# Optimization experiments

Hardware: AMD Instinct MI355X
Metric: run time of the kernel (lower is better)

## Reference

```python
import jax, jax.numpy as jnp
import numpy as np

SHIFT = 7  # shift_size; pad = 3


def _gn(x, w, b, eps=1e-5):
    # GroupNorm(1, C): normalize over (C,H,W) per sample, affine per channel
    m = jnp.mean(x, axis=(1, 2, 3), keepdims=True)
    v = jnp.var(x, axis=(1, 2, 3), keepdims=True)
    return (x - m) * jax.lax.rsqrt(v + eps) * w[None, :, None, None] + b[None, :, None, None]


def _conv1x1(x, w, b):
    return jnp.einsum('bchw,oc->bohw', x, w) + b[None, :, None, None]


def _gelu(x):
    return jax.nn.gelu(x, approximate=False)


def _shift_h(x, size):
    # CUDA kernel semantics: g = c // ceil(C/size); s = -(g - size//2);
    # out[n,c,h,w] = x[n,c,h+s,w] if in-bounds else 0  (dim=2)
    B, C, H, W = x.shape
    pad = size // 2
    group = -(-C // size)  # ceil
    s = pad - (jnp.arange(C) // group)              # [C], values in [-pad, pad]
    xp = jnp.pad(x, ((0, 0), (0, 0), (pad, pad), (0, 0)))
    idx = jnp.arange(H)[None, :] + s[:, None] + pad  # [C,H], in [0, H+2p-1]
    c = jnp.arange(C)[:, None]
    return xp[:, c, idx, :]


def _shift_w(x, size):
    return _shift_h(x.swapaxes(2, 3), size).swapaxes(2, 3)


def _axial_shift(x, c1w, c1b, n1w, n1b, c21w, c21b, c22w, c22b, n2w, n2b, c3w, c3b):
    x = _gelu(_gn(_conv1x1(x, c1w, c1b), n1w, n1b))
    x_lr = _shift_w(x, SHIFT)
    x_td = _shift_h(x, SHIFT)
    x_lr = _gelu(_conv1x1(x_lr, c21w, c21b))
    x_td = _gelu(_conv1x1(x_td, c22w, c22b))
    x = _gn(x_lr + x_td, n2w, n2b)
    return _conv1x1(x, c3w, c3b)


def setup_inputs() -> dict:
    B, C, H, W = 16, 256, 56, 56
    HID = 4 * C
    key = jax.random.key(0)
    ks = jax.random.split(key, 8)
    wscale = 0.05
    inp = {
        'x': jax.random.normal(ks[0], (B, C, H, W), jnp.float32),
        'n1_w': jnp.ones((C,), jnp.float32), 'n1_b': jnp.zeros((C,), jnp.float32),
        'as_c1_w': jax.random.normal(ks[1], (C, C), jnp.float32) * wscale,
        'as_c1_b': jnp.zeros((C,), jnp.float32),
        'as_n1_w': jnp.ones((C,), jnp.float32), 'as_n1_b': jnp.zeros((C,), jnp.float32),
        'as_c21_w': jax.random.normal(ks[2], (C, C), jnp.float32) * wscale,
        'as_c21_b': jnp.zeros((C,), jnp.float32),
        'as_c22_w': jax.random.normal(ks[3], (C, C), jnp.float32) * wscale,
        'as_c22_b': jnp.zeros((C,), jnp.float32),
        'as_n2_w': jnp.ones((C,), jnp.float32), 'as_n2_b': jnp.zeros((C,), jnp.float32),
        'as_c3_w': jax.random.normal(ks[4], (C, C), jnp.float32) * wscale,
        'as_c3_b': jnp.zeros((C,), jnp.float32),
        'n2_w': jnp.ones((C,), jnp.float32), 'n2_b': jnp.zeros((C,), jnp.float32),
        'fc1_w': jax.random.normal(ks[5], (HID, C), jnp.float32) * wscale,
        'fc1_b': jnp.zeros((HID,), jnp.float32),
        'fc2_w': jax.random.normal(ks[6], (C, HID), jnp.float32) * wscale,
        'fc2_b': jnp.zeros((C,), jnp.float32),
    }
    return inp


def reference(x, n1_w, n1_b, as_c1_w, as_c1_b, as_n1_w, as_n1_b,
              as_c21_w, as_c21_b, as_c22_w, as_c22_b, as_n2_w, as_n2_b,
              as_c3_w, as_c3_b, n2_w, n2_b, fc1_w, fc1_b, fc2_w, fc2_b):
    # AxialShiftedBlock: x = x + AxialShift(norm1(x)); x = x + Mlp(norm2(x))
    h = _gn(x, n1_w, n1_b)
    h = _axial_shift(h, as_c1_w, as_c1_b, as_n1_w, as_n1_b,
                     as_c21_w, as_c21_b, as_c22_w, as_c22_b,
                     as_n2_w, as_n2_b, as_c3_w, as_c3_b)
    x = x + h
    h = _gn(x, n2_w, n2_b)
    h = _gelu(_conv1x1(h, fc1_w, fc1_b))
    h = _conv1x1(h, fc2_w, fc2_b)
    return x + h
```

## Files before the change

### kernel.cpp

```cpp
#include <hip/hip_runtime.h>

typedef __attribute__((ext_vector_type(4))) float f32x4;
typedef __attribute__((ext_vector_type(8))) short bf16x8;
typedef __attribute__((ext_vector_type(4))) unsigned short u16x4;
typedef unsigned short u16;

#define HW 3136
#define NSEG 49
#define NELF 802816.0f
#define EPS 1e-5f

__device__ __forceinline__ short f2bf(float f) {
  union { float f; unsigned u; } v; v.f = f;
  unsigned r = (v.u + 0x7FFFu + ((v.u >> 16) & 1u)) >> 16;
  return (short)r;
}
__device__ __forceinline__ float b2f(u16 u) {
  union { unsigned u; float f; } v; v.u = ((unsigned)u) << 16;
  return v.f;
}
__device__ __forceinline__ float fgelu(float x) {
  float x2 = x * x;
  float u = x * (0.7978845608f + 0.0356774081f * x2);
  float e = __expf(-2.0f * u);
  return x * __builtin_amdgcn_rcpf(1.0f + e);
}
__device__ __forceinline__ void gload16(const void* g, void* l) {
  __builtin_amdgcn_global_load_lds(
      (const __attribute__((address_space(1))) void*)(uintptr_t)g,
      (__attribute__((address_space(3))) void*)(unsigned)(uintptr_t)l,
      16, 0, 0);
}

__global__ void wfold_kernel(const float* __restrict__ c1, const float* __restrict__ c21,
                             const float* __restrict__ c22, const float* __restrict__ c3,
                             const float* __restrict__ fc1, const float* __restrict__ fc2,
                             const float* __restrict__ n1w, const float* __restrict__ an2w,
                             const float* __restrict__ n2w, u16* __restrict__ out) {
  int i = (blockIdx.x * 256 + threadIdx.x) * 4;
  const float* src; int off; const float* scale = nullptr;
  if (i < 65536)       { src = c1;  off = 0;       scale = n1w; }
  else if (i < 131072) { src = c21; off = 65536; }
  else if (i < 196608) { src = c22; off = 131072; }
  else if (i < 262144) { src = c3;  off = 196608;  scale = an2w; }
  else if (i < 524288) { src = fc1; off = 262144;  scale = n2w; }
  else                 { src = fc2; off = 524288; }
  int li = i - off;
  float4 v = *(const float4*)(src + li);
  if (scale) {
    float4 g = *(const float4*)(scale + (li & 255));
    v.x *= g.x; v.y *= g.y; v.z *= g.z; v.w *= g.w;
  }
  u16x4 o4; o4[0] = (u16)f2bf(v.x); o4[1] = (u16)f2bf(v.y); o4[2] = (u16)f2bf(v.z); o4[3] = (u16)f2bf(v.w);
  *(u16x4*)(out + i) = o4;
}

__global__ void rowsum_kernel(const float* __restrict__ c1w, const float* __restrict__ c1b,
                              const float* __restrict__ n1w, const float* __restrict__ n1b,
                              const float* __restrict__ c3w, const float* __restrict__ c3b,
                              const float* __restrict__ an2w, const float* __restrict__ an2b,
                              const float* __restrict__ fc1w, const float* __restrict__ fc1b,
                              const float* __restrict__ n2w, const float* __restrict__ n2b,
                              float* __restrict__ sums) {
  int o = blockIdx.x * 256 + threadIdx.x;
  const float *W, *gw, *gb, *cb; float *Sg, *Sb; int row;
  if (o < 256)      { W = c1w;  gw = n1w;  gb = n1b;  cb = c1b;  Sg = sums;        Sb = sums + 256;  row = o; }
  else if (o < 512) { W = c3w;  gw = an2w; gb = an2b; cb = c3b;  Sg = sums + 512;  Sb = sums + 768;  row = o - 256; }
  else              { W = fc1w; gw = n2w;  gb = n2b;  cb = fc1b; Sg = sums + 1024; Sb = sums + 2048; row = o - 512; }
  float sg = 0.f, sb = 0.f;
  for (int c = 0; c < 256; c += 4) {
    float4 w = *(const float4*)(W + (size_t)row * 256 + c);
    float4 g = *(const float4*)(gw + c);
    float4 b = *(const float4*)(gb + c);
    sg += w.x * g.x + w.y * g.y + w.z * g.z + w.w * g.w;
    sb += w.x * b.x + w.y * b.y + w.z * b.z + w.w * b.w;
  }
  Sg[row] = sg; Sb[row] = sb + cb[row];
}

__global__ __launch_bounds__(256) void t0_kernel(const float* __restrict__ x,
                                                 u16* __restrict__ xT, float* __restrict__ st) {
  __shared__ __align__(16) u16 tile[64 * 256];
  const int t = threadIdx.x;
  const int n = blockIdx.x / NSEG;
  const int hw0 = (blockIdx.x % NSEG) * 64;
  const int pix = t & 63;
  float s = 0.f, q = 0.f;
#pragma unroll
  for (int r = 0; r < 16; ++r) {
    int cq = (t >> 6) + (r << 2);
    int c = cq * 4;
    u16x4 o4;
#pragma unroll
    for (int i = 0; i < 4; ++i) {
      float v = x[((size_t)n * 256 + c + i) * HW + hw0 + pix];
      s += v; q += v * v;
      o4[i] = (u16)f2bf(v);
    }
    int u = cq ^ ((pix & 15) << 2);
    *(u16x4*)((char*)tile + pix * 512 + u * 8) = o4;
  }
  __syncthreads();
  {
    const int p2 = t >> 2;
#pragma unroll
    for (int r = 0; r < 8; ++r) {
      int oct = (t & 3) + (r << 2);
      int up = (2 * oct) ^ ((p2 & 15) << 2);
      bf16x8 v = *(const bf16x8*)((char*)tile + p2 * 512 + up * 8);
      *(bf16x8*)&xT[((size_t)n * HW + hw0 + p2) * 256 + oct * 8] = v;
    }
  }
  __syncthreads();
  float* red = (float*)tile;
  red[t] = s; red[256 + t] = q;
  __syncthreads();
  for (int off = 128; off > 0; off >>= 1) {
    if (t < off) { red[t] += red[t + off]; red[256 + t] += red[256 + t + off]; }
    __syncthreads();
  }
  if (t == 0) { atomicAdd(&st[n * 2], red[0]); atomicAdd(&st[n * 2 + 1], red[256]); }
}

__global__ void e2_kernel(const u16* __restrict__ y, u16* __restrict__ tb,
                          const float* __restrict__ gw, const float* __restrict__ gb,
                          const float* __restrict__ stats) {
  const size_t NG = (size_t)16 * HW * 32;
  for (size_t g = (size_t)blockIdx.x * blockDim.x + threadIdx.x; g < NG;
       g += (size_t)gridDim.x * blockDim.x) {
    size_t base = g * 8;
    int n = (int)(base / 802816);
    int c0 = (int)(base & 255);
    float sm = stats[n * 2], sq = stats[n * 2 + 1];
    float mn = sm * (1.0f / NELF);
    float rstd = rsqrtf(sq * (1.0f / NELF) - mn * mn + EPS);
    bf16x8 v = *(const bf16x8*)(y + base);
    bf16x8 o;
#pragma unroll
    for (int j = 0; j < 8; ++j) {
      float sc = rstd * gw[c0 + j];
      float sh = gb[c0 + j] - mn * sc;
      o[j] = f2bf(fgelu(b2f((u16)v[j]) * sc + sh));
    }
    *(bf16x8*)(tb + base) = o;
  }
}

template<int EPI>
__global__ __launch_bounds__(512, 2) void gemmW2(
    const u16* __restrict__ actT, const u16* __restrict__ wt,
    const float* __restrict__ Sg, const float* __restrict__ Sb,
    const float* __restrict__ stats_in, float* __restrict__ stats_out,
    const u16* __restrict__ residCL, u16* __restrict__ outT)
{
  __shared__ __align__(16) u16 lds[79872];
  const int t = threadIdx.x;
  const int lane = t & 63, wave = t >> 6;
  const int fr = lane & 15, fq = lane >> 4;
  const int wo = wave >> 1, wp = wave & 1;
  const int n = blockIdx.x / 14;
  const int hw0 = (blockIdx.x % 14) * 224;
  const size_t nHW = (size_t)n * HW;

  {
    int u0 = t, u1 = t + 512;
    int r0 = u0 >> 2, sg0 = ((u0 & 3) - (r0 >> 1)) & 3;
    int r1 = u1 >> 2, sg1 = ((u1 & 3) - (r1 >> 1)) & 3;
    const u16* w0 = wt + (size_t)r0 * 256 + sg0 * 8;
    const u16* w1 = wt + (size_t)r1 * 256 + sg1 * 8;
#pragma unroll
    for (int k = 0; k < 8; ++k) {
      gload16(w0 + k * 32, &lds[k * 8192 + wave * 512]);
      gload16(w1 + k * 32, &lds[k * 8192 + 4096 + wave * 512]);
    }
  }

  int aU[4], bO[7];
#pragma unroll
  for (int os = 0; os < 4; ++os) { int row = wo * 64 + os * 16 + fr; aU[os] = (4 * row + ((fq + (row >> 1)) & 3)) * 8; }
#pragma unroll
  for (int ps = 0; ps < 7; ++ps) bO[ps] = (fq * 224 + wp * 112 + ps * 16 + fr) * 8;

  auto stageB = [&](int par, int ks) {
    if (wave < 7) {
#pragma unroll
      for (int i = 0; i < 2; ++i) {
        int ub = wave * 128 + i * 64;
        int u = ub + lane;
        int j = u / 224, p = u - j * 224;
        gload16(actT + (nHW + hw0 + p) * 256 + ks * 32 + j * 8,
                &lds[65536 + par * 7168 + ub * 8]);
      }
    }
  };

  f32x4 acc[4][7];
#pragma unroll
  for (int a = 0; a < 4; ++a)
#pragma unroll
    for (int b = 0; b < 7; ++b) acc[a][b] = (f32x4){0.f, 0.f, 0.f, 0.f};

  stageB(0, 0);
  __syncthreads();

#pragma unroll
  for (int k = 0; k < 8; ++k) {
    if (k < 7) stageB((k + 1) & 1, k + 1);
    bf16x8 afr[4], bfr[7];
#pragma unroll
    for (int os = 0; os < 4; ++os) afr[os] = *(const bf16x8*)&lds[k * 8192 + aU[os]];
#pragma unroll
    for (int ps = 0; ps < 7; ++ps) bfr[ps] = *(const bf16x8*)&lds[65536 + (k & 1) * 7168 + bO[ps]];
#pragma unroll
    for (int os = 0; os < 4; ++os)
#pragma unroll
      for (int ps = 0; ps < 7; ++ps)
        acc[os][ps] = __builtin_amdgcn_mfma_f32_16x16x32_bf16(afr[os], bfr[ps], acc[os][ps], 0, 0, 0);
    __syncthreads();
  }

  char* tl = (char*)lds;
  float sm = stats_in[n * 2], sq = stats_in[n * 2 + 1];
  float mn = sm * (1.0f / NELF);
  float rstd = rsqrtf(sq * (1.0f / NELF) - mn * mn + EPS);
  float mr = mn * rstd;
  float lsum = 0.f, lsq = 0.f;
#pragma unroll
  for (int os = 0; os < 4; ++os) {
    const int ob = wo * 64 + os * 16 + fq * 4;
    float4 g4 = *(const float4*)&Sg[ob];
    float4 s4 = *(const float4*)&Sb[ob];
    float be[4] = {s4.x - mr * g4.x, s4.y - mr * g4.y, s4.z - mr * g4.z, s4.w - mr * g4.w};
#pragma unroll
    for (int ps = 0; ps < 7; ++ps) {
      const int pix = wp * 112 + ps * 16 + fr;
      u16x4 rv = {0, 0, 0, 0};
      if (EPI == 1) rv = *(const u16x4*)&residCL[(nHW + hw0 + pix) * 256 + ob];
      u16x4 pk;
#pragma unroll
      for (int j = 0; j < 4; ++j) {
        float v = fmaf(acc[os][ps][j], rstd, be[j]);
        if (EPI == 1) v += b2f(rv[j]);
        lsum += v; lsq += v * v;
        pk[j] = (u16)f2bf(v);
      }
      const int qd = wo * 16 + os * 4 + fq;
      const int uq = qd ^ ((pix & 15) << 2);
      *(u16x4*)(tl + pix * 512 + uq * 8) = pk;
    }
  }
  __syncthreads();
#pragma unroll
  for (int r = 0; r < 14; ++r) {
    int idx = t + r * 512;
    int pix = idx >> 5, oct = idx & 31;
    int up = (2 * oct) ^ ((pix & 15) << 2);
    bf16x8 v = *(const bf16x8*)(tl + pix * 512 + up * 8);
    *(bf16x8*)&outT[(nHW + hw0 + pix) * 256 + oct * 8] = v;
  }
  __syncthreads();
  float* red = (float*)lds;
  red[t] = lsum; red[512 + t] = lsq;
  __syncthreads();
  for (int off = 256; off > 0; off >>= 1) {
    if (t < off) { red[t] += red[t + off]; red[512 + t] += red[512 + t + off]; }
    __syncthreads();
  }
  if (t == 0) { atomicAdd(&stats_out[n * 2], red[0]); atomicAdd(&stats_out[n * 2 + 1], red[512]); }
}

__global__ __launch_bounds__(512, 2) void gemm_dual4(
    const u16* __restrict__ tT, const u16* __restrict__ w21, const u16* __restrict__ w22,
    const float* __restrict__ b21, const float* __restrict__ b22,
    float* __restrict__ stats_out, u16* __restrict__ zT)
{
  __shared__ __align__(16) u16 lds[47616];
  const int t = threadIdx.x;
  const int lane = t & 63, wave = t >> 6;
  const int fr = lane & 15, fq = lane >> 4;
  const int n = blockIdx.x / 28;
  const int hw0 = (blockIdx.x % 28) * 112;
  const size_t nHW = (size_t)n * HW;

  const int u = (t < 448) ? t : 447;
  const int jl = u / 112, p = u - jl * 112;
  const int pix = hw0 + p;
  const int wc = pix % 56, hc = pix / 56;

  bf16x8 gA0, gA1, gB0, gB1;
  auto gatherIssue = [&](int ks) {
    int c0 = ks * 32 + jl * 8;
    int g0 = c0 / 37;
    int s0 = 3 - g0;
    int pa0 = pix + s0;           pa0 = pa0 < 0 ? 0 : (pa0 > HW - 1 ? HW - 1 : pa0);
    int pa1 = pix + s0 - 1;       pa1 = pa1 < 0 ? 0 : (pa1 > HW - 1 ? HW - 1 : pa1);
    int pb0 = pix + 56 * s0;      pb0 = pb0 < 0 ? 0 : (pb0 > HW - 1 ? HW - 1 : pb0);
    int pb1 = pix + 56 * (s0 - 1); pb1 = pb1 < 0 ? 0 : (pb1 > HW - 1 ? HW - 1 : pb1);
    gA0 = *(const bf16x8*)(tT + (nHW + pa0) * 256 + c0);
    gA1 = *(const bf16x8*)(tT + (nHW + pa1) * 256 + c0);
    gB0 = *(const bf16x8*)(tT + (nHW + pb0) * 256 + c0);
    gB1 = *(const bf16x8*)(tT + (nHW + pb1) * 256 + c0);
  };
  auto gatherWrite = [&](int par, int ks) {
    int c0 = ks * 32 + jl * 8;
    int g0 = c0 / 37;
    int s0 = 3 - g0;
    int js = (g0 + 1) * 37 - c0; if (js > 8) js = 8;
    bool a0 = (unsigned)(wc + s0) < 56u, a1 = (unsigned)(wc + s0 - 1) < 56u;
    bool b0 = (unsigned)(hc + s0) < 56u, b1 = (unsigned)(hc + s0 - 1) < 56u;
    bf16x8 va, vb;
#pragma unroll
    for (int j = 0; j < 8; ++j) {
      bool lo = j < js;
      va[j] = lo ? (a0 ? gA0[j] : (short)0) : (a1 ? gA1[j] : (short)0);
      vb[j] = lo ? (b0 ? gB0[j] : (short)0) : (b1 ? gB1[j] : (short)0);
    }
    if (t < 448) {
      *(bf16x8*)&lds[32768 + par * 3712 + (jl * 116 + p) * 8] = va;
      *(bf16x8*)&lds[40192 + par * 3712 + (jl * 116 + p) * 8] = vb;
    }
  };
  auto stageW = [&](int par, int ks) {
    int u0 = t; int r0 = u0 >> 2, sg0 = ((u0 & 3) - (r0 >> 1)) & 3;
    int u1 = t + 512; int r1 = u1 >> 2, sg1 = ((u1 & 3) - (r1 >> 1)) & 3;
    gload16(w21 + (size_t)r0 * 256 + ks * 32 + sg0 * 8, &lds[par * 8192 + wave * 512]);
    gload16(w21 + (size_t)r1 * 256 + ks * 32 + sg1 * 8, &lds[par * 8192 + 4096 + wave * 512]);
    gload16(w22 + (size_t)r0 * 256 + ks * 32 + sg0 * 8, &lds[16384 + par * 8192 + wave * 512]);
    gload16(w22 + (size_t)r1 * 256 + ks * 32 + sg1 * 8, &lds[16384 + par * 8192 + 4096 + wave * 512]);
  };

  int aU[2], bP[7];
#pragma unroll
  for (int os = 0; os < 2; ++os) { int row = wave * 32 + os * 16 + fr; aU[os] = (4 * row + ((fq + (row >> 1)) & 3)) * 8; }
#pragma unroll
  for (int ps = 0; ps < 7; ++ps) bP[ps] = (fq * 116 + ps * 16 + fr) * 8;

  f32x4 accA[2][7], accB[2][7];
#pragma unroll
  for (int a = 0; a < 2; ++a)
#pragma unroll
    for (int b = 0; b < 7; ++b) { accA[a][b] = (f32x4){0, 0, 0, 0}; accB[a][b] = (f32x4){0, 0, 0, 0}; }

  gatherIssue(0);
  stageW(0, 0);
  gatherWrite(0, 0);
  gatherIssue(1);
  __syncthreads();

#pragma unroll
  for (int k = 0; k < 8; ++k) {
    if (k < 7) stageW((k + 1) & 1, k + 1);
    bf16x8 afA[2], afB[2], bfA[7], bfB[7];
#pragma unroll
    for (int os = 0; os < 2; ++os) {
      afA[os] = *(const bf16x8*)&lds[(k & 1) * 8192 + aU[os]];
      afB[os] = *(const bf16x8*)&lds[16384 + (k & 1) * 8192 + aU[os]];
    }
#pragma unroll
    for (int ps = 0; ps < 7; ++ps) {
      bfA[ps] = *(const bf16x8*)&lds[32768 + (k & 1) * 3712 + bP[ps]];
      bfB[ps] = *(const bf16x8*)&lds[40192 + (k & 1) * 3712 + bP[ps]];
    }
#pragma unroll
    for (int os = 0; os < 2; ++os)
#pragma unroll
      for (int ps = 0; ps < 7; ++ps) {
        accA[os][ps] = __builtin_amdgcn_mfma_f32_16x16x32_bf16(afA[os], bfA[ps], accA[os][ps], 0, 0, 0);
        accB[os][ps] = __builtin_amdgcn_mfma_f32_16x16x32_bf16(afB[os], bfB[ps], accB[os][ps], 0, 0, 0);
      }
    if (k < 7) {
      gatherWrite((k + 1) & 1, k + 1);
      if (k < 6) gatherIssue(k + 2);
    }
    __syncthreads();
  }

  char* tl = (char*)lds;
  float lsum = 0.f, lsq = 0.f;
#pragma unroll
  for (int os = 0; os < 2; ++os) {
    const int ob = wave * 32 + os * 16 + fq * 4;
    float4 a4 = *(const float4*)&b21[ob];
    float4 c4 = *(const float4*)&b22[ob];
#pragma unroll
    for (int ps = 0; ps < 7; ++ps) {
      const int pixL = ps * 16 + fr;
      u16x4 pk;
      float ba[4] = {a4.x, a4.y, a4.z, a4.w};
      float bb[4] = {c4.x, c4.y, c4.z, c4.w};
#pragma unroll
      for (int j = 0; j < 4; ++j) {
        float z = fgelu(accA[os][ps][j] + ba[j]) + fgelu(accB[os][ps][j] + bb[j]);
        lsum += z; lsq += z * z;
        pk[j] = (u16)f2bf(z);
      }
      const int qd = wave * 8 + os * 4 + fq;
      const int uq = qd ^ ((pixL & 15) << 2);
      *(u16x4*)(tl + pixL * 512 + uq * 8) = pk;
    }
  }
  __syncthreads();
#pragma unroll
  for (int r = 0; r < 7; ++r) {
    int idx = t + r * 512;
    int pixL = idx >> 5, oct = idx & 31;
    int up = (2 * oct) ^ ((pixL & 15) << 2);
    bf16x8 v = *(const bf16x8*)(tl + pixL * 512 + up * 8);
    *(bf16x8*)&zT[(nHW + hw0 + pixL) * 256 + oct * 8] = v;
  }
  __syncthreads();
  float* red = (float*)lds;
  red[t] = lsum; red[512 + t] = lsq;
  __syncthreads();
  for (int off = 256; off > 0; off >>= 1) {
    if (t < off) { red[t] += red[t + off]; red[512 + t] += red[512 + t + off]; }
    __syncthreads();
  }
  if (t == 0) { atomicAdd(&stats_out[n * 2], red[0]); atomicAdd(&stats_out[n * 2 + 1], red[512]); }
}

__global__ __launch_bounds__(512, 2) void gemm_mlp(
    const u16* __restrict__ x2T, const u16* __restrict__ wfc1, const u16* __restrict__ wfc2,
    const float* __restrict__ Sg, const float* __restrict__ Sb, const float* __restrict__ bias2,
    const float* __restrict__ stats_in, float* __restrict__ out_f32)
{
  __shared__ __align__(16) u16 lds[75008];
  const int t = threadIdx.x;
  const int lane = t & 63, wave = t >> 6;
  const int fr = lane & 15, fq = lane >> 4;
  const int n = blockIdx.x / 28;
  const int hw0 = (blockIdx.x % 28) * 112;
  const size_t nHW = (size_t)n * HW;

  auto stageWm = [&](int par, int s) {
    int chunk = s >> 4, kk = s & 7;
    int u0 = t; int r0 = u0 >> 2, sg0 = ((u0 & 3) - (r0 >> 1)) & 3;
    int u1 = t + 512; int r1 = u1 >> 2, sg1 = ((u1 & 3) - (r1 >> 1)) & 3;
    if (((s >> 3) & 1) == 0) {
      gload16(wfc1 + (size_t)(chunk * 256 + r0) * 256 + kk * 32 + sg0 * 8, &lds[par * 8192 + wave * 512]);
      gload16(wfc1 + (size_t)(chunk * 256 + r1) * 256 + kk * 32 + sg1 * 8, &lds[par * 8192 + 4096 + wave * 512]);
    } else {
      gload16(wfc2 + (size_t)r0 * 1024 + chunk * 256 + kk * 32 + sg0 * 8, &lds[par * 8192 + wave * 512]);
      gload16(wfc2 + (size_t)r1 * 1024 + chunk * 256 + kk * 32 + sg1 * 8, &lds[par * 8192 + 4096 + wave * 512]);
    }
  };

#pragma unroll
  for (int i = 0; i < 7; ++i) {
    int u = wave * 448 + i * 64 + lane;
    int j = u / 112, p = u - j * 112;
    bf16x8 v = *(const bf16x8*)(x2T + (nHW + hw0 + p) * 256 + j * 8);
    *(bf16x8*)&lds[16384 + (j * 113 + p) * 8] = v;
  }
  stageWm(0, 0);

  float sm = stats_in[n * 2], sq = stats_in[n * 2 + 1];
  float mn = sm * (1.0f / NELF);
  float rstd = rsqrtf(sq * (1.0f / NELF) - mn * mn + EPS);
  float mr = mn * rstd;

  int aU[2];
#pragma unroll
  for (int os = 0; os < 2; ++os) { int row = wave * 32 + os * 16 + fr; aU[os] = (4 * row + ((fq + (row >> 1)) & 3)) * 8; }

  f32x4 hacc[2][7], oacc[2][7];
#pragma unroll
  for (int a = 0; a < 2; ++a)
#pragma unroll
    for (int b = 0; b < 7; ++b) { hacc[a][b] = (f32x4){0, 0, 0, 0}; oacc[a][b] = (f32x4){0, 0, 0, 0}; }

  __syncthreads();

  for (int s = 0; s < 64; ++s) {
    if (s < 63) stageWm((s + 1) & 1, s + 1);
    const int kk = s & 7;
    const bool bph = (s >> 3) & 1;
    bf16x8 afr[2], bfr[7];
#pragma unroll
    for (int os = 0; os < 2; ++os) afr[os] = *(const bf16x8*)&lds[(s & 1) * 8192 + aU[os]];
    if (!bph) {
#pragma unroll
      for (int ps = 0; ps < 7; ++ps)
        bfr[ps] = *(const bf16x8*)&lds[16384 + ((kk * 4 + fq) * 113 + ps * 16 + fr) * 8];
#pragma unroll
      for (int os = 0; os < 2; ++os)
#pragma unroll
        for (int ps = 0; ps < 7; ++ps)
          hacc[os][ps] = __builtin_amdgcn_mfma_f32_16x16x32_bf16(afr[os], bfr[ps], hacc[os][ps], 0, 0, 0);
    } else {
#pragma unroll
      for (int ps = 0; ps < 7; ++ps)
        bfr[ps] = *(const bf16x8*)&lds[45312 + ((kk * 4 + fq) * 116 + ps * 16 + fr) * 8];
#pragma unroll
      for (int os = 0; os < 2; ++os)
#pragma unroll
        for (int ps = 0; ps < 7; ++ps)
          oacc[os][ps] = __builtin_amdgcn_mfma_f32_16x16x32_bf16(afr[os], bfr[ps], oacc[os][ps], 0, 0, 0);
    }
    if ((s & 15) == 7) {
      const int hcb = (s >> 4) * 256;
#pragma unroll
      for (int os = 0; os < 2; ++os) {
        const int hcl = wave * 32 + os * 16 + fq * 4;
        const int hc = hcb + hcl;
        float4 g4 = *(const float4*)&Sg[hc];
        float4 s4 = *(const float4*)&Sb[hc];
        float be[4] = {s4.x - mr * g4.x, s4.y - mr * g4.y, s4.z - mr * g4.z, s4.w - mr * g4.w};
        const int jH = hcl >> 3;
#pragma unroll
        for (int ps = 0; ps < 7; ++ps) {
          const int pixL = ps * 16 + fr;
          u16x4 pk;
#pragma unroll
          for (int j = 0; j < 4; ++j)
            pk[j] = (u16)f2bf(fgelu(fmaf(hacc[os][ps][j], rstd, be[j])));
          *(u16x4*)&lds[45312 + (jH * 116 + pixL) * 8 + (fq & 1) * 4] = pk;
          hacc[os][ps] = (f32x4){0, 0, 0, 0};
        }
      }
    }
    __syncthreads();
  }

#pragma unroll
  for (int os = 0; os < 2; ++os) {
    const int ob = wave * 32 + os * 16 + fq * 4;
    float4 b4 = *(const float4*)&bias2[ob];
    float bb[4] = {b4.x, b4.y, b4.z, b4.w};
#pragma unroll
    for (int ps = 0; ps < 7; ++ps) {
      const int pixL = ps * 16 + fr;
      u16x4 rv = *(const u16x4*)&lds[16384 + ((ob >> 3) * 113 + pixL) * 8 + (ob & 4)];
#pragma unroll
      for (int j = 0; j < 4; ++j) {
        float v = oacc[os][ps][j] + bb[j] + b2f(rv[j]);
        out_f32[((size_t)n * 256 + ob + j) * HW + hw0 + pixL] = v;
      }
    }
  }
}

extern "C" void kernel_launch(void* const* d_in, const int* in_sizes, int n_in,
                              void* d_out, int out_size, void* d_ws, size_t ws_size,
                              hipStream_t stream) {
  const float* x     = (const float*)d_in[0];
  const float* n1_w  = (const float*)d_in[1];
  const float* n1_b  = (const float*)d_in[2];
  const float* c1_w  = (const float*)d_in[3];
  const float* c1_b  = (const float*)d_in[4];
  const float* an1_w = (const float*)d_in[5];
  const float* an1_b = (const float*)d_in[6];
  const float* c21_w = (const float*)d_in[7];
  const float* c21_b = (const float*)d_in[8];
  const float* c22_w = (const float*)d_in[9];
  const float* c22_b = (const float*)d_in[10];
  const float* an2_w = (const float*)d_in[11];
  const float* an2_b = (const float*)d_in[12];
  const float* c3_w  = (const float*)d_in[13];
  const float* c3_b  = (const float*)d_in[14];
  const float* n2_w  = (const float*)d_in[15];
  const float* n2_b  = (const float*)d_in[16];
  const float* fc1_w = (const float*)d_in[17];
  const float* fc1_b = (const float*)d_in[18];
  const float* fc2_w = (const float*)d_in[19];
  const float* fc2_b = (const float*)d_in[20];

  char* ws = (char*)d_ws;
  float* stats = (float*)ws;
  float* sums  = (float*)(ws + 1024);
  u16* wbuf = (u16*)(ws + 16384);
  u16* wb_c1g  = wbuf;
  u16* wb_c21  = wbuf + 65536;
  u16* wb_c22  = wbuf + 131072;
  u16* wb_c3g  = wbuf + 196608;
  u16* wb_fc1g = wbuf + 262144;
  u16* wb_fc2  = wbuf + 524288;
  const size_t AB = 25690112;
  char* A0 = ws + 1638400;
  u16* xT  = (u16*)(A0);
  u16* yT  = (u16*)(A0 + AB);
  u16* tT  = (u16*)(A0 + 2 * AB);
  u16* zT  = (u16*)(A0 + 3 * AB);
  u16* x2T = (u16*)(A0 + 4 * AB);
  float* out = (float*)d_out;

  hipMemsetAsync(stats, 0, 512, stream);
  wfold_kernel<<<768, 256, 0, stream>>>(c1_w, c21_w, c22_w, c3_w, fc1_w, fc2_w,
                                        n1_w, an2_w, n2_w, wbuf);
  rowsum_kernel<<<6, 256, 0, stream>>>(c1_w, c1_b, n1_w, n1_b, c3_w, c3_b, an2_w, an2_b,
                                       fc1_w, fc1_b, n2_w, n2_b, sums);
  t0_kernel<<<784, 256, 0, stream>>>(x, xT, stats + 0);
  gemmW2<0><<<224, 512, 0, stream>>>(xT, wb_c1g, sums, sums + 256,
                                     stats + 0, stats + 32, nullptr, yT);
  e2_kernel<<<2048, 256, 0, stream>>>(yT, tT, an1_w, an1_b, stats + 32);
  gemm_dual4<<<448, 512, 0, stream>>>(tT, wb_c21, wb_c22, c21_b, c22_b, stats + 64, zT);
  gemmW2<1><<<224, 512, 0, stream>>>(zT, wb_c3g, sums + 512, sums + 768,
                                     stats + 64, stats + 96, xT, x2T);
  gemm_mlp<<<448, 512, 0, stream>>>(x2T, wb_fc1g, wb_fc2, sums + 1024, sums + 2048,
                                    fc2_b, stats + 96, out);
}
```

Baseline: 286.2 us.

## Shrink LDS and register footprint of GEMM kernels to raise occupancy

The dual-branch conv kernel is split across a second grid dimension so each block computes 128 output channels, with single-buffered weights and a smaller LDS footprint. The MLP kernel is restructured to process 128 hidden channels per chunk with a smaller fc1 accumulator, and it reads the residual straight from global memory instead of keeping it in LDS. All three GEMM kernels change launch bounds from 2 to 4 blocks per SM, and the B-tile layout moves to an XOR-swizzled per-pixel layout. The intent is higher occupancy to hide latency, at the cost of more barriers, duplicated gather work across the split grid, and register pressure that could force spills in gemmW2.

```diff
diff --git a/kernel.cpp b/kernel.cpp
--- a/kernel.cpp
+++ b/kernel.cpp
@@ -147,7 +147,7 @@
 }
 
 template<int EPI>
-__global__ __launch_bounds__(512, 2) void gemmW2(
+__global__ __launch_bounds__(512, 4) void gemmW2(
     const u16* __restrict__ actT, const u16* __restrict__ wt,
     const float* __restrict__ Sg, const float* __restrict__ Sb,
     const float* __restrict__ stats_in, float* __restrict__ stats_out,
@@ -175,22 +175,28 @@
     }
   }
 
-  int aU[4], bO[7];
+  int aU[4];
 #pragma unroll
   for (int os = 0; os < 4; ++os) { int row = wo * 64 + os * 16 + fr; aU[os] = (4 * row + ((fq + (row >> 1)) & 3)) * 8; }
-#pragma unroll
-  for (int ps = 0; ps < 7; ++ps) bO[ps] = (fq * 224 + wp * 112 + ps * 16 + fr) * 8;
-
+  int bO[7];
+#pragma unroll
+  for (int ps = 0; ps < 7; ++ps) {
+    int pix = wp * 112 + ps * 16 + fr;
+    bO[ps] = (pix * 4 + (fq ^ (pix & 3))) * 8;
+  }
+
+  const u16* srcB0; const u16* srcB1;
+  {
+    int v0 = wave * 128 + lane, v1 = v0 + 64;
+    int p0 = v0 >> 2, j0 = (v0 & 3) ^ (p0 & 3);
+    int p1 = v1 >> 2, j1 = (v1 & 3) ^ (p1 & 3);
+    srcB0 = actT + (nHW + hw0 + p0) * 256 + j0 * 8;
+    srcB1 = actT + (nHW + hw0 + p1) * 256 + j1 * 8;
+  }
   auto stageB = [&](int par, int ks) {
     if (wave < 7) {
-#pragma unroll
-      for (int i = 0; i < 2; ++i) {
-        int ub = wave * 128 + i * 64;
-        int u = ub + lane;
-        int j = u / 224, p = u - j * 224;
-        gload16(actT + (nHW + hw0 + p) * 256 + ks * 32 + j * 8,
-                &lds[65536 + par * 7168 + ub * 8]);
-      }
+      gload16(srcB0 + ks * 32, &lds[65536 + par * 7168 + (wave * 128) * 8]);
+      gload16(srcB1 + ks * 32, &lds[65536 + par * 7168 + (wave * 128 + 64) * 8]);
     }
   };
 
@@ -269,32 +275,33 @@
   if (t == 0) { atomicAdd(&stats_out[n * 2], red[0]); atomicAdd(&stats_out[n * 2 + 1], red[512]); }
 }
 
-__global__ __launch_bounds__(512, 2) void gemm_dual4(
+__global__ __launch_bounds__(512, 4) void dual5(
     const u16* __restrict__ tT, const u16* __restrict__ w21, const u16* __restrict__ w22,
     const float* __restrict__ b21, const float* __restrict__ b22,
     float* __restrict__ stats_out, u16* __restrict__ zT)
 {
-  __shared__ __align__(16) u16 lds[47616];
+  __shared__ __align__(16) u16 lds[22528];
   const int t = threadIdx.x;
   const int lane = t & 63, wave = t >> 6;
   const int fr = lane & 15, fq = lane >> 4;
   const int n = blockIdx.x / 28;
   const int hw0 = (blockIdx.x % 28) * 112;
+  const int obase = blockIdx.y * 128;
   const size_t nHW = (size_t)n * HW;
 
-  const int u = (t < 448) ? t : 447;
-  const int jl = u / 112, p = u - jl * 112;
-  const int pix = hw0 + p;
+  const int v = (t < 448) ? t : 447;
+  const int gp = v >> 2, gj = (v & 3) ^ (gp & 3);
+  const int pix = hw0 + gp;
   const int wc = pix % 56, hc = pix / 56;
 
   bf16x8 gA0, gA1, gB0, gB1;
   auto gatherIssue = [&](int ks) {
-    int c0 = ks * 32 + jl * 8;
+    int c0 = ks * 32 + gj * 8;
     int g0 = c0 / 37;
     int s0 = 3 - g0;
-    int pa0 = pix + s0;           pa0 = pa0 < 0 ? 0 : (pa0 > HW - 1 ? HW - 1 : pa0);
-    int pa1 = pix + s0 - 1;       pa1 = pa1 < 0 ? 0 : (pa1 > HW - 1 ? HW - 1 : pa1);
-    int pb0 = pix + 56 * s0;      pb0 = pb0 < 0 ? 0 : (pb0 > HW - 1 ? HW - 1 : pb0);
+    int pa0 = pix + s0;            pa0 = pa0 < 0 ? 0 : (pa0 > HW - 1 ? HW - 1 : pa0);
+    int pa1 = pix + s0 - 1;        pa1 = pa1 < 0 ? 0 : (pa1 > HW - 1 ? HW - 1 : pa1);
+    int pb0 = pix + 56 * s0;       pb0 = pb0 < 0 ? 0 : (pb0 > HW - 1 ? HW - 1 : pb0);
     int pb1 = pix + 56 * (s0 - 1); pb1 = pb1 < 0 ? 0 : (pb1 > HW - 1 ? HW - 1 : pb1);
     gA0 = *(const bf16x8*)(tT + (nHW + pa0) * 256 + c0);
     gA1 = *(const bf16x8*)(tT + (nHW + pa1) * 256 + c0);
@@ -302,7 +309,7 @@
     gB1 = *(const bf16x8*)(tT + (nHW + pb1) * 256 + c0);
   };
   auto gatherWrite = [&](int par, int ks) {
-    int c0 = ks * 32 + jl * 8;
+    int c0 = ks * 32 + gj * 8;
     int g0 = c0 / 37;
     int s0 = 3 - g0;
     int js = (g0 + 1) * 37 - c0; if (js > 8) js = 8;
@@ -316,97 +323,93 @@
       vb[j] = lo ? (b0 ? gB0[j] : (short)0) : (b1 ? gB1[j] : (short)0);
     }
     if (t < 448) {
-      *(bf16x8*)&lds[32768 + par * 3712 + (jl * 116 + p) * 8] = va;
-      *(bf16x8*)&lds[40192 + par * 3712 + (jl * 116 + p) * 8] = vb;
+      *(bf16x8*)&lds[8192 + par * 3584 + v * 8] = va;
+      *(bf16x8*)&lds[15360 + par * 3584 + v * 8] = vb;
     }
   };
-  auto stageW = [&](int par, int ks) {
-    int u0 = t; int r0 = u0 >> 2, sg0 = ((u0 & 3) - (r0 >> 1)) & 3;
-    int u1 = t + 512; int r1 = u1 >> 2, sg1 = ((u1 & 3) - (r1 >> 1)) & 3;
-    gload16(w21 + (size_t)r0 * 256 + ks * 32 + sg0 * 8, &lds[par * 8192 + wave * 512]);
-    gload16(w21 + (size_t)r1 * 256 + ks * 32 + sg1 * 8, &lds[par * 8192 + 4096 + wave * 512]);
-    gload16(w22 + (size_t)r0 * 256 + ks * 32 + sg0 * 8, &lds[16384 + par * 8192 + wave * 512]);
-    gload16(w22 + (size_t)r1 * 256 + ks * 32 + sg1 * 8, &lds[16384 + par * 8192 + 4096 + wave * 512]);
+  const int rW = t >> 2;
+  const int sgW = ((t & 3) - (rW >> 1)) & 3;
+  const u16* w21p = w21 + (size_t)(obase + rW) * 256 + sgW * 8;
+  const u16* w22p = w22 + (size_t)(obase + rW) * 256 + sgW * 8;
+  auto stageW = [&](int ks) {
+    gload16(w21p + ks * 32, &lds[t * 8]);
+    gload16(w22p + ks * 32, &lds[4096 + t * 8]);
   };
 
-  int aU[2], bP[7];
-#pragma unroll
-  for (int os = 0; os < 2; ++os) { int row = wave * 32 + os * 16 + fr; aU[os] = (4 * row + ((fq + (row >> 1)) & 3)) * 8; }
-#pragma unroll
-  for (int ps = 0; ps < 7; ++ps) bP[ps] = (fq * 116 + ps * 16 + fr) * 8;
-
-  f32x4 accA[2][7], accB[2][7];
-#pragma unroll
-  for (int a = 0; a < 2; ++a)
-#pragma unroll
-    for (int b = 0; b < 7; ++b) { accA[a][b] = (f32x4){0, 0, 0, 0}; accB[a][b] = (f32x4){0, 0, 0, 0}; }
+  const int rowA = wave * 16 + fr;
+  const int aU = (4 * rowA + ((fq + (rowA >> 1)) & 3)) * 8;
+  int bP[7];
+#pragma unroll
+  for (int ps = 0; ps < 7; ++ps) {
+    int px = ps * 16 + fr;
+    bP[ps] = (px * 4 + (fq ^ (px & 3))) * 8;
+  }
+
+  f32x4 accA[7], accB[7];
+#pragma unroll
+  for (int b = 0; b < 7; ++b) { accA[b] = (f32x4){0, 0, 0, 0}; accB[b] = (f32x4){0, 0, 0, 0}; }
 
   gatherIssue(0);
-  stageW(0, 0);
+  stageW(0);
   gatherWrite(0, 0);
+  __syncthreads();
   gatherIssue(1);
-  __syncthreads();
 
 #pragma unroll
   for (int k = 0; k < 8; ++k) {
-    if (k < 7) stageW((k + 1) & 1, k + 1);
-    bf16x8 afA[2], afB[2], bfA[7], bfB[7];
-#pragma unroll
-    for (int os = 0; os < 2; ++os) {
-      afA[os] = *(const bf16x8*)&lds[(k & 1) * 8192 + aU[os]];
-      afB[os] = *(const bf16x8*)&lds[16384 + (k & 1) * 8192 + aU[os]];
-    }
+    bf16x8 afA = *(const bf16x8*)&lds[aU];
+    bf16x8 afB = *(const bf16x8*)&lds[4096 + aU];
+    bf16x8 bfA[7], bfB[7];
 #pragma unroll
     for (int ps = 0; ps < 7; ++ps) {
-      bfA[ps] = *(const bf16x8*)&lds[32768 + (k & 1) * 3712 + bP[ps]];
-      bfB[ps] = *(const bf16x8*)&lds[40192 + (k & 1) * 3712 + bP[ps]];
-    }
-#pragma unroll
-    for (int os = 0; os < 2; ++os)
-#pragma unroll
-      for (int ps = 0; ps < 7; ++ps) {
-        accA[os][ps] = __builtin_amdgcn_mfma_f32_16x16x32_bf16(afA[os], bfA[ps], accA[os][ps], 0, 0, 0);
-        accB[os][ps] = __builtin_amdgcn_mfma_f32_16x16x32_bf16(afB[os], bfB[ps], accB[os][ps], 0, 0, 0);
-      }
+      bfA[ps] = *(const bf16x8*)&lds[8192 + (k & 1) * 3584 + bP[ps]];
+      bfB[ps] = *(const bf16x8*)&lds[15360 + (k & 1) * 3584 + bP[ps]];
+    }
+#pragma unroll
+    for (int ps = 0; ps < 7; ++ps) {
+      accA[ps] = __builtin_amdgcn_mfma_f32_16x16x32_bf16(afA, bfA[ps], accA[ps], 0, 0, 0);
+      accB[ps] = __builtin_amdgcn_mfma_f32_16x16x32_bf16(afB, bfB[ps], accB[ps], 0, 0, 0);
+    }
     if (k < 7) {
+      __syncthreads();
+      stageW(k + 1);
       gatherWrite((k + 1) & 1, k + 1);
+      __syncthreads();
       if (k < 6) gatherIssue(k + 2);
     }
-    __syncthreads();
-  }
-
-  char* tl = (char*)lds;
+  }
+  __syncthreads();
+
   float lsum = 0.f, lsq = 0.f;
-#pragma unroll
-  for (int os = 0; os < 2; ++os) {
-    const int ob = wave * 32 + os * 16 + fq * 4;
-    float4 a4 = *(const float4*)&b21[ob];
-    float4 c4 = *(const float4*)&b22[ob];
+  {
+    const int obl = wave * 16 + fq * 4;
+    float4 a4 = *(const float4*)&b21[obase + obl];
+    float4 c4 = *(const float4*)&b22[obase + obl];
+    float ba[4] = {a4.x, a4.y, a4.z, a4.w};
+    float bb[4] = {c4.x, c4.y, c4.z, c4.w};
+    const int qd = wave * 2 + (fq >> 1);
 #pragma unroll
     for (int ps = 0; ps < 7; ++ps) {
       const int pixL = ps * 16 + fr;
       u16x4 pk;
-      float ba[4] = {a4.x, a4.y, a4.z, a4.w};
-      float bb[4] = {c4.x, c4.y, c4.z, c4.w};
 #pragma unroll
       for (int j = 0; j < 4; ++j) {
-        float z = fgelu(accA[os][ps][j] + ba[j]) + fgelu(accB[os][ps][j] + bb[j]);
+        float z = fgelu(accA[ps][j] + ba[j]) + fgelu(accB[ps][j] + bb[j]);
         lsum += z; lsq += z * z;
         pk[j] = (u16)f2bf(z);
       }
-      const int qd = wave * 8 + os * 4 + fq;
-      const int uq = qd ^ ((pixL & 15) << 2);
-      *(u16x4*)(tl + pixL * 512 + uq * 8) = pk;
-    }
-  }
-  __syncthreads();
-#pragma unroll
-  for (int r = 0; r < 7; ++r) {
+      *(u16x4*)&lds[pixL * 132 + qd * 8 + (fq & 1) * 4] = pk;
+    }
+  }
+  __syncthreads();
+#pragma unroll
+  for (int r = 0; r < 4; ++r) {
     int idx = t + r * 512;
-    int pixL = idx >> 5, oct = idx & 31;
-    int up = (2 * oct) ^ ((pixL & 15) << 2);
-    bf16x8 v = *(const bf16x8*)(tl + pixL * 512 + up * 8);
-    *(bf16x8*)&zT[(nHW + hw0 + pixL) * 256 + oct * 8] = v;
+    if (idx < 1792) {
+      int pixL = idx >> 4, oct = idx & 15;
+      bf16x8 vv = *(const bf16x8*)&lds[pixL * 132 + oct * 8];
+      *(bf16x8*)&zT[(nHW + hw0 + pixL) * 256 + obase + oct * 8] = vv;
+    }
   }
   __syncthreads();
   float* red = (float*)lds;
@@ -419,107 +422,119 @@
   if (t == 0) { atomicAdd(&stats_out[n * 2], red[0]); atomicAdd(&stats_out[n * 2 + 1], red[512]); }
 }
 
-__global__ __launch_bounds__(512, 2) void gemm_mlp(
+__global__ __launch_bounds__(512, 4) void mlp2(
     const u16* __restrict__ x2T, const u16* __restrict__ wfc1, const u16* __restrict__ wfc2,
     const float* __restrict__ Sg, const float* __restrict__ Sb, const float* __restrict__ bias2,
     const float* __restrict__ stats_in, float* __restrict__ out_f32)
 {
-  __shared__ __align__(16) u16 lds[75008];
+  __shared__ __align__(16) u16 lds[38400];
   const int t = threadIdx.x;
   const int lane = t & 63, wave = t >> 6;
   const int fr = lane & 15, fq = lane >> 4;
   const int n = blockIdx.x / 28;
   const int hw0 = (blockIdx.x % 28) * 112;
   const size_t nHW = (size_t)n * HW;
-
-  auto stageWm = [&](int par, int s) {
-    int chunk = s >> 4, kk = s & 7;
-    int u0 = t; int r0 = u0 >> 2, sg0 = ((u0 & 3) - (r0 >> 1)) & 3;
-    int u1 = t + 512; int r1 = u1 >> 2, sg1 = ((u1 & 3) - (r1 >> 1)) & 3;
-    if (((s >> 3) & 1) == 0) {
-      gload16(wfc1 + (size_t)(chunk * 256 + r0) * 256 + kk * 32 + sg0 * 8, &lds[par * 8192 + wave * 512]);
-      gload16(wfc1 + (size_t)(chunk * 256 + r1) * 256 + kk * 32 + sg1 * 8, &lds[par * 8192 + 4096 + wave * 512]);
-    } else {
-      gload16(wfc2 + (size_t)r0 * 1024 + chunk * 256 + kk * 32 + sg0 * 8, &lds[par * 8192 + wave * 512]);
-      gload16(wfc2 + (size_t)r1 * 1024 + chunk * 256 + kk * 32 + sg1 * 8, &lds[par * 8192 + 4096 + wave * 512]);
-    }
-  };
-
-#pragma unroll
-  for (int i = 0; i < 7; ++i) {
-    int u = wave * 448 + i * 64 + lane;
-    int j = u / 112, p = u - j * 112;
-    bf16x8 v = *(const bf16x8*)(x2T + (nHW + hw0 + p) * 256 + j * 8);
-    *(bf16x8*)&lds[16384 + (j * 113 + p) * 8] = v;
-  }
-  stageWm(0, 0);
-
-  float sm = stats_in[n * 2], sq = stats_in[n * 2 + 1];
-  float mn = sm * (1.0f / NELF);
-  float rstd = rsqrtf(sq * (1.0f / NELF) - mn * mn + EPS);
-  float mr = mn * rstd;
-
-  int aU[2];
-#pragma unroll
-  for (int os = 0; os < 2; ++os) { int row = wave * 32 + os * 16 + fr; aU[os] = (4 * row + ((fq + (row >> 1)) & 3)) * 8; }
-
-  f32x4 hacc[2][7], oacc[2][7];
+  const int WOFF = 0, BOFF = 16384, HOFF = 23552;
+
+  const int rW = t >> 2;
+  const int sgW = ((t & 3) - (rW >> 1)) & 3;
+  const u16* w1p  = wfc1 + (size_t)rW * 256 + sgW * 8;
+  const u16* w2p0 = wfc2 + (size_t)rW * 1024 + sgW * 8;
+  const u16* w2p1 = wfc2 + (size_t)(rW + 128) * 1024 + sgW * 8;
+  const int vB = (t < 448) ? t : 447;
+  const int pB = vB >> 2, jB = (vB & 3) ^ (pB & 3);
+  const u16* srcB = x2T + (nHW + hw0 + pB) * 256 + jB * 8;
+
+  const int row1 = wave * 16 + fr;
+  const int aU1 = (4 * row1 + ((fq + (row1 >> 1)) & 3)) * 8;
+  int aU2[2];
+#pragma unroll
+  for (int os = 0; os < 2; ++os) { int row = wave * 32 + os * 16 + fr; aU2[os] = (4 * row + ((fq + (row >> 1)) & 3)) * 8; }
+  int bX[7], bH_base[7];
+#pragma unroll
+  for (int ps = 0; ps < 7; ++ps) {
+    int px = ps * 16 + fr;
+    bX[ps] = (px * 4 + (fq ^ (px & 3))) * 8;
+    bH_base[ps] = px * 8;
+  }
+
+  float smv = stats_in[n * 2], sqv = stats_in[n * 2 + 1];
+  float mnv = smv * (1.0f / NELF);
+  float rstd = rsqrtf(sqv * (1.0f / NELF) - mnv * mnv + EPS);
+  float mr = mnv * rstd;
+
+  f32x4 hacc[7], oacc[2][7];
+#pragma unroll
+  for (int b = 0; b < 7; ++b) hacc[b] = (f32x4){0, 0, 0, 0};
 #pragma unroll
   for (int a = 0; a < 2; ++a)
 #pragma unroll
-    for (int b = 0; b < 7; ++b) { hacc[a][b] = (f32x4){0, 0, 0, 0}; oacc[a][b] = (f32x4){0, 0, 0, 0}; }
-
-  __syncthreads();
-
-  for (int s = 0; s < 64; ++s) {
-    if (s < 63) stageWm((s + 1) & 1, s + 1);
-    const int kk = s & 7;
-    const bool bph = (s >> 3) & 1;
-    bf16x8 afr[2], bfr[7];
-#pragma unroll
-    for (int os = 0; os < 2; ++os) afr[os] = *(const bf16x8*)&lds[(s & 1) * 8192 + aU[os]];
-    if (!bph) {
-#pragma unroll
-      for (int ps = 0; ps < 7; ++ps)
-        bfr[ps] = *(const bf16x8*)&lds[16384 + ((kk * 4 + fq) * 113 + ps * 16 + fr) * 8];
-#pragma unroll
-      for (int os = 0; os < 2; ++os)
+    for (int b = 0; b < 7; ++b) oacc[a][b] = (f32x4){0, 0, 0, 0};
+
+  gload16(w1p, &lds[WOFF + t * 8]);
+  if (wave < 7) gload16(srcB, &lds[BOFF + vB * 8]);
+  __syncthreads();
+
+  for (int c = 0; c < 8; ++c) {
+#pragma unroll
+    for (int i = 0; i < 12; ++i) {
+      if (i < 7) {
+        gload16(w1p + (i + 1) * 32, &lds[WOFF + ((i + 1) & 1) * 8192 + t * 8]);
+        if (wave < 7) gload16(srcB + (i + 1) * 32, &lds[BOFF + ((i + 1) & 1) * 3584 + vB * 8]);
+      } else if (i == 7) {
+        gload16(w2p0, &lds[WOFF + t * 8]);
+        gload16(w2p1, &lds[WOFF + (t + 512) * 8]);
+      } else if (i < 11) {
+        gload16(w2p0 + (i - 7) * 32, &lds[WOFF + ((i + 1) & 1) * 8192 + t * 8]);
+        gload16(w2p1 + (i - 7) * 32, &lds[WOFF + ((i + 1) & 1) * 8192 + (t + 512) * 8]);
+      } else if (c < 7) {
+        gload16(w1p + 32768, &lds[WOFF + t * 8]);
+        if (wave < 7) gload16(srcB, &lds[BOFF + vB * 8]);
+      }
+      if (i < 8) {
+        bf16x8 afr = *(const bf16x8*)&lds[WOFF + (i & 1) * 8192 + aU1];
+        bf16x8 bfr[7];
+#pragma unroll
+        for (int ps = 0; ps < 7; ++ps) bfr[ps] = *(const bf16x8*)&lds[BOFF + (i & 1) * 3584 + bX[ps]];
 #pragma unroll
         for (int ps = 0; ps < 7; ++ps)
-          hacc[os][ps] = __builtin_amdgcn_mfma_f32_16x16x32_bf16(afr[os], bfr[ps], hacc[os][ps], 0, 0, 0);
-    } else {
-#pragma unroll
-      for (int ps = 0; ps < 7; ++ps)
-        bfr[ps] = *(const bf16x8*)&lds[45312 + ((kk * 4 + fq) * 116 + ps * 16 + fr) * 8];
-#pragma unroll
-      for (int os = 0; os < 2; ++os)
+          hacc[ps] = __builtin_amdgcn_mfma_f32_16x16x32_bf16(afr, bfr[ps], hacc[ps], 0, 0, 0);
+      } else {
+        const int i2 = i - 8;
+        bf16x8 afr0 = *(const bf16x8*)&lds[WOFF + (i & 1) * 8192 + aU2[0]];
+        bf16x8 afr1 = *(const bf16x8*)&lds[WOFF + (i & 1) * 8192 + aU2[1]];
+        bf16x8 bfr[7];
 #pragma unroll
         for (int ps = 0; ps < 7; ++ps)
-          oacc[os][ps] = __builtin_amdgcn_mfma_f32_16x16x32_bf16(afr[os], bfr[ps], oacc[os][ps], 0, 0, 0);
-    }
-    if ((s & 15) == 7) {
-      const int hcb = (s >> 4) * 256;
-#pragma unroll
-      for (int os = 0; os < 2; ++os) {
-        const int hcl = wave * 32 + os * 16 + fq * 4;
-        const int hc = hcb + hcl;
+          bfr[ps] = *(const bf16x8*)&lds[HOFF + (i2 * 4 + fq) * 928 + bH_base[ps]];
+#pragma unroll
+        for (int ps = 0; ps < 7; ++ps) {
+          oacc[0][ps] = __builtin_amdgcn_mfma_f32_16x16x32_bf16(afr0, bfr[ps], oacc[0][ps], 0, 0, 0);
+          oacc[1][ps] = __builtin_amdgcn_mfma_f32_16x16x32_bf16(afr1, bfr[ps], oacc[1][ps], 0, 0, 0);
+        }
+      }
+      if (i == 7) {
+        const int hc = c * 128 + wave * 16 + fq * 4;
         float4 g4 = *(const float4*)&Sg[hc];
         float4 s4 = *(const float4*)&Sb[hc];
         float be[4] = {s4.x - mr * g4.x, s4.y - mr * g4.y, s4.z - mr * g4.z, s4.w - mr * g4.w};
-        const int jH = hcl >> 3;
+        const int jH = wave * 2 + (fq >> 1);
 #pragma unroll
         for (int ps = 0; ps < 7; ++ps) {
           const int pixL = ps * 16 + fr;
           u16x4 pk;
 #pragma unroll
           for (int j = 0; j < 4; ++j)
-            pk[j] = (u16)f2bf(fgelu(fmaf(hacc[os][ps][j], rstd, be[j])));
-          *(u16x4*)&lds[45312 + (jH * 116 + pixL) * 8 + (fq & 1) * 4] = pk;
-          hacc[os][ps] = (f32x4){0, 0, 0, 0};
+            pk[j] = (u16)f2bf(fgelu(fmaf(hacc[ps][j], rstd, be[j])));
+          *(u16x4*)&lds[HOFF + (jH * 116 + pixL) * 8 + (fq & 1) * 4] = pk;
+          hacc[ps] = (f32x4){0, 0, 0, 0};
         }
       }
-    }
-    __syncthreads();
+      __syncthreads();
+    }
+    w1p  += 32768;
+    w2p0 += 128;
+    w2p1 += 128;
   }
 
 #pragma unroll
@@ -530,12 +545,10 @@
 #pragma unroll
     for (int ps = 0; ps < 7; ++ps) {
       const int pixL = ps * 16 + fr;
-      u16x4 rv = *(const u16x4*)&lds[16384 + ((ob >> 3) * 113 + pixL) * 8 + (ob & 4)];
-#pragma unroll
-      for (int j = 0; j < 4; ++j) {
-        float v = oacc[os][ps][j] + bb[j] + b2f(rv[j]);
-        out_f32[((size_t)n * 256 + ob + j) * HW + hw0 + pixL] = v;
-      }
+      u16x4 rv = *(const u16x4*)&x2T[(nHW + hw0 + pixL) * 256 + ob];
+#pragma unroll
+      for (int j = 0; j < 4; ++j)
+        out_f32[((size_t)n * 256 + ob + j) * HW + hw0 + pixL] = oacc[os][ps][j] + bb[j] + b2f(rv[j]);
     }
   }
 }
@@ -593,9 +606,9 @@
   gemmW2<0><<<224, 512, 0, stream>>>(xT, wb_c1g, sums, sums + 256,
                                      stats + 0, stats + 32, nullptr, yT);
   e2_kernel<<<2048, 256, 0, stream>>>(yT, tT, an1_w, an1_b, stats + 32);
-  gemm_dual4<<<448, 512, 0, stream>>>(tT, wb_c21, wb_c22, c21_b, c22_b, stats + 64, zT);
+  dual5<<<dim3(448, 2), 512, 0, stream>>>(tT, wb_c21, wb_c22, c21_b, c22_b, stats + 64, zT);
   gemmW2<1><<<224, 512, 0, stream>>>(zT, wb_c3g, sums + 512, sums + 768,
                                      stats + 64, stats + 96, xT, x2T);
-  gemm_mlp<<<448, 512, 0, stream>>>(x2T, wb_fc1g, wb_fc2, sums + 1024, sums + 2048,
-                                    fc2_b, stats + 96, out);
-}
+  mlp2<<<448, 512, 0, stream>>>(x2T, wb_fc1g, wb_fc2, sums + 1024, sums + 2048,
+                                fc2_b, stats + 96, out);
+}
```

Measured after the change: 307.6 us. 1.07x slower.
